# Optimization experiments

Measured on AMD Instinct MI355X. Metric: run time of the kernel, lower is better.

Reference implementation:

```python
import jax, jax.numpy as jnp
import numpy as np

C = 256          # in_dim
DQK = C // 16    # query/key channels after 1x1 conv


def setup_inputs() -> dict:
    key = jax.random.key(0)
    ks = jax.random.split(key, 10)
    B, W, H = 8, 64, 64
    s = 0.02
    return {
        "x1": jax.random.normal(ks[0], (B, C, W, H), jnp.float32),
        "x2": jax.random.normal(ks[1], (B, C, W, H), jnp.float32),
        "Wq": jax.random.normal(ks[2], (DQK, 2 * C), jnp.float32) * s,
        "bq": jnp.zeros((DQK,), jnp.float32),
        "Wk": jax.random.normal(ks[3], (DQK, 2 * C), jnp.float32) * s,
        "bk": jnp.zeros((DQK,), jnp.float32),
        "Wv1": jax.random.normal(ks[4], (C, C), jnp.float32) * s,
        "bv1": jnp.zeros((C,), jnp.float32),
        "Wv2": jax.random.normal(ks[5], (C, C), jnp.float32) * s,
        "bv2": jnp.zeros((C,), jnp.float32),
    }


def reference(x1, x2, Wq, bq, Wk, bk, Wv1, bv1, Wv2, bv2):
    B, c, W, H = x1.shape
    N = W * H
    x = jnp.concatenate([x1, x2], axis=1)            # [B, 2C, W, H]
    xf = x.reshape(B, 2 * c, N)                      # flatten spatial
    # 1x1 convs == channel matmuls
    q = jnp.einsum('dc,bcn->bnd', Wq, xf) + bq       # [B, N, DQK]
    k = jnp.einsum('dc,bcn->bdn', Wk, xf) + bk[None, :, None]  # [B, DQK, N]
    energy = jnp.einsum('bnd,bdm->bnm', q, k)        # [B, N, N]
    attention = jax.nn.softmax(energy, axis=-1)
    x1f = x1.reshape(B, c, N)
    x2f = x2.reshape(B, c, N)
    v1 = jnp.einsum('oc,bcn->bon', Wv1, x1f) + bv1[None, :, None]
    v2 = jnp.einsum('oc,bcn->bon', Wv2, x2f) + bv2[None, :, None]
    # bmm(value, attention^T): out[b,c,n] = sum_m v[b,c,m] * attention[b,n,m]
    out1 = jnp.einsum('bcm,bnm->bcn', v1, attention).reshape(B, c, W, H) + x1
    out2 = jnp.einsum('bcm,bnm->bcn', v2, attention).reshape(B, c, W, H) + x2
    return out1, out2, attention
```

## Files before the change

### kernel.cpp

```cpp
#include <hip/hip_runtime.h>
#include <hip/hip_bf16.h>

#define B_ 8
#define C_ 256
#define N_ 4096
#define D_ 16
#define TWO_C 512

#define PSLOT_SHORTS 4128
#define PSLOT_BYTES  (PSLOT_SHORTS * 2)

typedef __bf16 bf16x8 __attribute__((ext_vector_type(8)));
typedef __bf16 bf16x4 __attribute__((ext_vector_type(4)));
typedef float f32x4 __attribute__((ext_vector_type(4)));
typedef unsigned short u16x4 __attribute__((ext_vector_type(4)));

static __device__ __forceinline__ unsigned short f2bf_rtn(float f) {
    unsigned int u = __builtin_bit_cast(unsigned int, f);
    u += 0x7fffu + ((u >> 16) & 1u);
    return (unsigned short)(u >> 16);
}

static __device__ __forceinline__ float bf2f(unsigned short s) {
    return __builtin_bit_cast(float, (unsigned int)s << 16);
}

__device__ __forceinline__ void gld16(const void* g, void* l) {
    __builtin_amdgcn_global_load_lds(
        (const __attribute__((address_space(1))) unsigned int*)g,
        (__attribute__((address_space(3))) unsigned int*)l, 16, 0, 0);
}

__device__ __forceinline__ f32x4 expv(f32x4 e) {
    f32x4 r = { __expf(e[0]), __expf(e[1]), __expf(e[2]), __expf(e[3]) };
    return r;
}

#define MF(K, Q) __builtin_amdgcn_mfma_f32_16x16x32_bf16((K), (Q), zerov, 0, 0, 0)

__global__ __launch_bounds__(256) void wconv(
    const float* __restrict__ Wv1, const float* __restrict__ Wv2,
    unsigned short* __restrict__ Wbf)
{
    const int i = blockIdx.x * 256 + threadIdx.x;
    f32x4 a = ((const f32x4*)Wv1)[i];
    f32x4 b = ((const f32x4*)Wv2)[i];
    u16x4 ua = { f2bf_rtn(a[0]), f2bf_rtn(a[1]), f2bf_rtn(a[2]), f2bf_rtn(a[3]) };
    u16x4 ub = { f2bf_rtn(b[0]), f2bf_rtn(b[1]), f2bf_rtn(b[2]), f2bf_rtn(b[3]) };
    ((u16x4*)Wbf)[i] = ua;
    ((u16x4*)Wbf)[16384 + i] = ub;
}

__global__ __launch_bounds__(256) void qk_part(
    const float* __restrict__ x1, const float* __restrict__ x2,
    const float* __restrict__ Wq, const float* __restrict__ Wk,
    float* __restrict__ pq, float* __restrict__ pk,
    unsigned short* __restrict__ xbfT)
{
    const int tid = threadIdx.x;
    const int bid = blockIdx.x;
    const int ch = bid & 3;
    const int nt = (bid >> 2) & 15;
    const int b  = bid >> 6;
    const int n  = nt * 256 + tid;

    const float* xs  = (ch < 2) ? x1 : x2;
    const int xoff = (ch & 1) * 128;
    const int wcol = ch * 128;

    const float* px = xs + ((size_t)b * C_ + xoff) * N_ + n;
    unsigned short* xT = xbfT + ((size_t)b * N_ + n) * TWO_C + wcol;

    float aq[D_], ak[D_];
#pragma unroll
    for (int d = 0; d < D_; ++d) { aq[d] = 0.f; ak[d] = 0.f; }

    for (int c8 = 0; c8 < 16; ++c8) {
        unsigned short xb[8];
#pragma unroll
        for (int j = 0; j < 8; ++j) {
            const int c = c8 * 8 + j;
            float xv = px[(size_t)c * N_];
            xb[j] = f2bf_rtn(xv);
#pragma unroll
            for (int d = 0; d < D_; ++d) {
                aq[d] += Wq[d * TWO_C + wcol + c] * xv;
                ak[d] += Wk[d * TWO_C + wcol + c] * xv;
            }
        }
        u16x4 lo = { xb[0], xb[1], xb[2], xb[3] };
        u16x4 hi = { xb[4], xb[5], xb[6], xb[7] };
        *(u16x4*)(xT + c8 * 8)     = lo;
        *(u16x4*)(xT + c8 * 8 + 4) = hi;
    }

    f32x4* q4 = (f32x4*)pq + (size_t)ch * B_ * N_ * 4 + ((size_t)b * N_ + n) * 4;
    f32x4* k4 = (f32x4*)pk + (size_t)ch * B_ * N_ * 4 + ((size_t)b * N_ + n) * 4;
#pragma unroll
    for (int j = 0; j < 4; ++j) {
        f32x4 tq = { aq[4*j], aq[4*j+1], aq[4*j+2], aq[4*j+3] };
        f32x4 tk = { ak[4*j], ak[4*j+1], ak[4*j+2], ak[4*j+3] };
        q4[j] = tq;
        k4[j] = tk;
    }
}

__global__ __launch_bounds__(256) void qk_reduce(
    const float* __restrict__ pq, const float* __restrict__ pk,
    const float* __restrict__ bq, const float* __restrict__ bk,
    unsigned short* __restrict__ qbf, unsigned short* __restrict__ kbf)
{
    const int tg = blockIdx.x * 256 + threadIdx.x;
    const int row = tg >> 2;
    const int d4  = tg & 3;
    const f32x4* pq4 = (const f32x4*)pq;
    const f32x4* pk4 = (const f32x4*)pk;
    f32x4 q = ((const f32x4*)bq)[d4];
    f32x4 k = ((const f32x4*)bk)[d4];
    const size_t stride = (size_t)B_ * N_ * 4;
#pragma unroll
    for (int ch = 0; ch < 4; ++ch) {
        q += pq4[ch * stride + tg];
        k += pk4[ch * stride + tg];
    }
    u16x4 qo = { f2bf_rtn(q[0]), f2bf_rtn(q[1]), f2bf_rtn(q[2]), f2bf_rtn(q[3]) };
    u16x4 ko = { f2bf_rtn(k[0]), f2bf_rtn(k[1]), f2bf_rtn(k[2]), f2bf_rtn(k[3]) };
    u16x4 z  = { 0, 0, 0, 0 };
    *(u16x4*)(qbf + (size_t)row * 32 + d4 * 4)      = qo;
    *(u16x4*)(qbf + (size_t)row * 32 + 16 + d4 * 4) = z;
    *(u16x4*)(kbf + (size_t)row * 32 + d4 * 4)      = ko;
    *(u16x4*)(kbf + (size_t)row * 32 + 16 + d4 * 4) = z;
}

__global__ __launch_bounds__(256) void v_mfma(
    const unsigned short* __restrict__ Wbf,
    const unsigned short* __restrict__ xbfT,
    const float* __restrict__ bv1, const float* __restrict__ bv2,
    unsigned short* __restrict__ vstack)
{
    const int tid  = threadIdx.x;
    const int lane = tid & 63;
    const int wid  = tid >> 6;
    const int bid  = blockIdx.x;
    const int b    = bid >> 7;
    const int half = (bid >> 6) & 1;
    const int n0   = (bid & 63) * 64;
    const int col  = lane & 15;
    const int grp  = lane >> 4;
    const int koff = grp * 8;

    const unsigned short* pa[4];
    const unsigned short* pb[4];
#pragma unroll
    for (int ai = 0; ai < 4; ++ai)
        pa[ai] = Wbf + (size_t)(half * 256 + wid * 64 + ai * 16 + col) * 256 + koff;
#pragma unroll
    for (int bj = 0; bj < 4; ++bj)
        pb[bj] = xbfT + ((size_t)b * N_ + n0 + bj * 16 + col) * TWO_C + half * 256 + koff;

    f32x4 acc[4][4];
#pragma unroll
    for (int ai = 0; ai < 4; ++ai)
#pragma unroll
        for (int bj = 0; bj < 4; ++bj)
            acc[ai][bj] = (f32x4){0.f, 0.f, 0.f, 0.f};

#pragma unroll
    for (int s = 0; s < 8; ++s) {
        bf16x8 af[4], bfr[4];
#pragma unroll
        for (int ai = 0; ai < 4; ++ai) af[ai] = *(const bf16x8*)(pa[ai] + s * 32);
#pragma unroll
        for (int bj = 0; bj < 4; ++bj) bfr[bj] = *(const bf16x8*)(pb[bj] + s * 32);
#pragma unroll
        for (int ai = 0; ai < 4; ++ai)
#pragma unroll
            for (int bj = 0; bj < 4; ++bj)
                acc[ai][bj] = __builtin_amdgcn_mfma_f32_16x16x32_bf16(
                    af[ai], bfr[bj], acc[ai][bj], 0, 0, 0);
    }

    const float* bias = half ? bv2 : bv1;
#pragma unroll
    for (int ai = 0; ai < 4; ++ai) {
        const int cb = wid * 64 + ai * 16 + grp * 4;
#pragma unroll
        for (int r = 0; r < 4; ++r) {
            const float bv = bias[cb + r];
            unsigned short* vr = vstack + ((size_t)b * 512 + half * 256 + cb + r) * N_;
#pragma unroll
            for (int bj = 0; bj < 4; ++bj)
                vr[n0 + bj * 16 + col] = f2bf_rtn(acc[ai][bj][r] + bv);
        }
    }
}

__global__ __launch_bounds__(256) void rowsum(
    const unsigned short* __restrict__ qbf,
    const unsigned short* __restrict__ kbf,
    float* __restrict__ sinvbuf)
{
    const int tid  = threadIdx.x;
    const int lane = tid & 63;
    const int wid  = tid >> 6;
    const int b  = blockIdx.x >> 6;
    const int n0 = (blockIdx.x & 63) * 64 + wid * 16;
    const int col = lane & 15;
    const int grp = lane >> 4;
    const f32x4 zerov = {0.f, 0.f, 0.f, 0.f};

    const bf16x8 qf = *(const bf16x8*)(qbf + ((size_t)b * N_ + n0 + col) * 32 + grp * 8);
    const unsigned short* kp = kbf + ((size_t)b * N_ + col) * 32 + grp * 8;

    float rs = 0.f;
#pragma unroll 4
    for (int t = 0; t < 128; ++t) {
        bf16x8 k0 = *(const bf16x8*)kp;
        bf16x8 k1 = *(const bf16x8*)(kp + 512);
        kp += 1024;
        f32x4 p0 = expv(MF(k0, qf));
        f32x4 p1 = expv(MF(k1, qf));
        rs += (p0[0] + p0[1]) + (p0[2] + p0[3])
            + (p1[0] + p1[1]) + (p1[2] + p1[3]);
    }
    rs += __shfl_xor(rs, 16);
    rs += __shfl_xor(rs, 32);
    if (lane < 16)
        sinvbuf[(size_t)b * N_ + n0 + col] = 1.f / rs;
}

__global__ __launch_bounds__(512) void fused_pv(
    const unsigned short* __restrict__ qbf,
    const unsigned short* __restrict__ kbf,
    const unsigned short* __restrict__ vstack,
    const float* __restrict__ sinvbuf,
    const float* __restrict__ x1, const float* __restrict__ x2,
    float* __restrict__ out1, float* __restrict__ out2,
    float* __restrict__ att)
{
    __shared__ unsigned short AsmR[3][256 * 32];
    __shared__ unsigned short Bring[3][PSLOT_SHORTS];
    __shared__ float sinvLds[128];

    const int tid  = threadIdx.x;
    const int lane = tid & 63;
    const int wid  = tid >> 6;
    const int wr   = wid >> 2;
    const int wc   = wid & 3;
    const int col  = lane & 15;
    const int grp  = lane >> 4;

    const int bid  = blockIdx.x;
    const int orig = (bid & 7) * 64 + (bid >> 3);
    const int b   = orig >> 6;
    const int idx = orig & 63;
    const int ct  = idx & 1;
    const int nt  = idx >> 1;
    const int n0  = nt * 128;

    const f32x4 zerov = {0.f, 0.f, 0.f, 0.f};

    const int nl = wid * 16 + col;
    if (tid < 128) sinvLds[tid] = sinvbuf[(size_t)b * N_ + n0 + tid];

    const bf16x8 qf = *(const bf16x8*)(qbf + ((size_t)b * N_ + n0 + nl) * 32 + grp * 8);
    const unsigned short* kbase = kbf + ((size_t)b * N_ + col) * 32 + grp * 8;

    const unsigned short* Vb = vstack + ((size_t)b * 512 + ct * 256) * N_;
    const int q1 = tid + 512;
    const unsigned short* pa0g = Vb + (size_t)(tid >> 2) * N_ + (((tid & 3) ^ ((tid >> 2) & 3)) * 8);
    const unsigned short* pa1g = Vb + (size_t)(q1 >> 2) * N_ + (((q1 & 3) ^ ((q1 >> 2) & 3)) * 8);

    const int bwA = nl * 64 + ((((grp >> 1)) ^ (col & 3)) << 4) + (grp & 1) * 8;
    const int bwB = bwA ^ 32;

    const int raBase = (wr * 128 + col) * 64 + ((grp ^ (col & 3)) << 4);
    const int rbBase = (wc * 32  + col) * 64 + ((grp ^ (col & 3)) << 4);

    const int fj = lane >> 3;
    const int fu = (lane >> 1) & 3;
    const int fh = lane & 1;
    const int rlF = ct * 64 + wid * 8 + fj;
    const int flOff = rlF * 64 + ((fu ^ (fj & 3)) << 4) + fh * 8;
    float* const attF = att + (size_t)b * N_ * N_ + (size_t)(n0 + rlF) * N_ + (lane & 7) * 4;

    f32x4 acc[8][2];
#pragma unroll
    for (int ai = 0; ai < 8; ++ai)
#pragma unroll
        for (int bj = 0; bj < 2; ++bj)
            acc[ai][bj] = zerov;

#define PACKB(P, BASE, OFF) do {                                              \
    bf16x4 pkv = { (__bf16)(P)[0], (__bf16)(P)[1],                            \
                   (__bf16)(P)[2], (__bf16)(P)[3] };                          \
    *(bf16x4*)((char*)(BASE) + (OFF)) = pkv;                                  \
} while (0)

    unsigned short *aC = &AsmR[0][0], *aN = &AsmR[1][0], *aT = &AsmR[2][0];
    unsigned short *pPrev = &Bring[2][0], *pC = &Bring[0][0], *pN = &Bring[1][0];

    gld16(pa0g, aC + tid * 8);
    gld16(pa1g, aC + tid * 8 + 4096);
    gld16(pa0g + 32, aN + tid * 8);
    gld16(pa1g + 32, aN + tid * 8 + 4096);
    __builtin_amdgcn_sched_barrier(0);
    bf16x8 kA0, kA1, kB0, kB1;
    kA0 = *(const bf16x8*)kbase;
    kA1 = *(const bf16x8*)(kbase + 512);
    kB0 = *(const bf16x8*)(kbase + 1024);
    kB1 = *(const bf16x8*)(kbase + 1536);
    {
        f32x4 p0 = expv(MF(kA0, qf));
        f32x4 p1 = expv(MF(kA1, qf));
        PACKB(p0, pC, bwA);
        PACKB(p1, pC, bwB);
    }
    asm volatile("s_waitcnt lgkmcnt(0)" ::: "memory");
    __builtin_amdgcn_s_barrier();
    __builtin_amdgcn_sched_barrier(0);
    const float ivF = sinvLds[rlF];

    auto step = [&](const bf16x8& kc0, const bf16x8& kc1,
                    bf16x8& kn0, bf16x8& kn1, int T) {
        bf16x8 bfr[2], af0[4], af1[4];
#pragma unroll
        for (int bj = 0; bj < 2; ++bj)
            bfr[bj] = *(const bf16x8*)((const char*)pC + rbBase + bj * 1024);
#pragma unroll
        for (int ai = 0; ai < 4; ++ai)
            af0[ai] = *(const bf16x8*)((const char*)aC + raBase + ai * 1024);
        const int mt2 = (T + 2 < 128) ? T + 2 : 127;
        gld16(pa0g + (size_t)mt2 * 32, aT + tid * 8);
        gld16(pa1g + (size_t)mt2 * 32, aT + tid * 8 + 4096);
        __builtin_amdgcn_sched_barrier(0);
        {
            f32x4 e0 = MF(kc0, qf);
            f32x4 e1 = MF(kc1, qf);
            kn0 = *(const bf16x8*)(kbase + (size_t)mt2 * 1024);
            kn1 = *(const bf16x8*)(kbase + (size_t)mt2 * 1024 + 512);
            f32x4 p0 = expv(e0);
            f32x4 p1 = expv(e1);
            PACKB(p0, pN, bwA);
            PACKB(p1, pN, bwB);
        }
        if (T > 0) {
            u16x4 pb = *(const u16x4*)((const char*)pPrev + flOff);
            f32x4 pv = { bf2f(pb[0]) * ivF, bf2f(pb[1]) * ivF,
                         bf2f(pb[2]) * ivF, bf2f(pb[3]) * ivF };
            *(f32x4*)(attF + (size_t)(T - 1) * 32) = pv;
        }
#pragma unroll
        for (int ai = 0; ai < 4; ++ai)
#pragma unroll
            for (int bj = 0; bj < 2; ++bj)
                acc[ai][bj] = __builtin_amdgcn_mfma_f32_16x16x32_bf16(
                    af0[ai], bfr[bj], acc[ai][bj], 0, 0, 0);
#pragma unroll
        for (int ai = 0; ai < 4; ++ai)
            af1[ai] = *(const bf16x8*)((const char*)aC + raBase + (4 + ai) * 1024);
#pragma unroll
        for (int ai = 0; ai < 4; ++ai)
#pragma unroll
            for (int bj = 0; bj < 2; ++bj)
                acc[4 + ai][bj] = __builtin_amdgcn_mfma_f32_16x16x32_bf16(
                    af1[ai], bfr[bj], acc[4 + ai][bj], 0, 0, 0);
        asm volatile("s_waitcnt lgkmcnt(0)" ::: "memory");
        __builtin_amdgcn_s_barrier();
        __builtin_amdgcn_sched_barrier(0);
        unsigned short* t1 = aC; aC = aN; aN = aT; aT = t1;
        unsigned short* t2 = pPrev; pPrev = pC; pC = pN; pN = t2;
    };

    for (int tt = 0; tt < 64; ++tt) {
        step(kB0, kB1, kA0, kA1, 2 * tt);
        step(kA0, kA1, kB0, kB1, 2 * tt + 1);
    }

    {
        u16x4 pb = *(const u16x4*)((const char*)pPrev + flOff);
        f32x4 pv = { bf2f(pb[0]) * ivF, bf2f(pb[1]) * ivF,
                     bf2f(pb[2]) * ivF, bf2f(pb[3]) * ivF };
        *(f32x4*)(attF + (size_t)127 * 32) = pv;
    }

    float* outp     = ct ? out2 : out1;
    const float* xp = ct ? x2 : x1;
    float sc[2];
#pragma unroll
    for (int bj = 0; bj < 2; ++bj)
        sc[bj] = sinvLds[wc * 32 + bj * 16 + col];
#pragma unroll
    for (int ai = 0; ai < 8; ++ai) {
        const int c_l = wr * 128 + ai * 16 + grp * 4;
#pragma unroll
        for (int bj = 0; bj < 2; ++bj) {
            const int n = n0 + wc * 32 + bj * 16 + col;
#pragma unroll
            for (int r = 0; r < 4; ++r) {
                const size_t idx = ((size_t)b * C_ + c_l + r) * N_ + n;
                outp[idx] = acc[ai][bj][r] * sc[bj] + xp[idx];
            }
        }
    }
#undef PACKB
}

extern "C" void kernel_launch(void* const* d_in, const int* in_sizes, int n_in,
                              void* d_out, int out_size, void* d_ws, size_t ws_size,
                              hipStream_t stream)
{
    const float* x1  = (const float*)d_in[0];
    const float* x2  = (const float*)d_in[1];
    const float* Wq  = (const float*)d_in[2];
    const float* bq  = (const float*)d_in[3];
    const float* Wk  = (const float*)d_in[4];
    const float* bk  = (const float*)d_in[5];
    const float* Wv1 = (const float*)d_in[6];
    const float* bv1 = (const float*)d_in[7];
    const float* Wv2 = (const float*)d_in[8];
    const float* bv2 = (const float*)d_in[9];

    float* out  = (float*)d_out;
    float* out1 = out;
    float* out2 = out + (size_t)B_ * C_ * N_;
    float* att  = out + 2 * (size_t)B_ * C_ * N_;

    unsigned short* xbfT = (unsigned short*)att;

    char* ws = (char*)d_ws;
    unsigned short* qbf = (unsigned short*)ws;
    unsigned short* kbf = (unsigned short*)(ws + (size_t)2 * 1024 * 1024);
    unsigned short* vstack = (unsigned short*)(ws + (size_t)4 * 1024 * 1024);
    float* pq = (float*)(ws + (size_t)36 * 1024 * 1024);
    float* pk = (float*)(ws + (size_t)44 * 1024 * 1024);
    unsigned short* Wbf = (unsigned short*)(ws + (size_t)52 * 1024 * 1024);
    float* sinvbuf = (float*)(ws + (size_t)53 * 1024 * 1024);

    wconv<<<64, 256, 0, stream>>>(Wv1, Wv2, Wbf);
    qk_part<<<B_ * 16 * 4, 256, 0, stream>>>(x1, x2, Wq, Wk, pq, pk, xbfT);
    qk_reduce<<<(B_ * N_ * 4) / 256, 256, 0, stream>>>(pq, pk, bq, bk, qbf, kbf);
    rowsum<<<B_ * 64, 256, 0, stream>>>(qbf, kbf, sinvbuf);
    v_mfma<<<B_ * 2 * 64, 256, 0, stream>>>(Wbf, xbfT, bv1, bv2, vstack);
    fused_pv<<<512, 512, 0, stream>>>(qbf, kbf, vstack, sinvbuf, x1, x2, out1, out2, att);
}
```

Before: 507.1 us.

## Double query tile per block to 256 rows and batch attention stores

Each fused_pv block now covers 256 query positions instead of 128, so every V tile loaded from global is reused across twice as many outputs, and the grid shrinks from 512 to 256 blocks. The P ring grows to six slots, and attention-matrix writes are batched every four steps from older slots, giving wider, more coalesced stores. The cost is a larger accumulator array (32 MFMA tiles per wave), more LDS, and fewer blocks than the 256 CUs can absorb, so occupancy and latency hiding may suffer.

After: 481.5 us. 1.05x faster.

```diff
diff --git a/kernel.cpp b/kernel.cpp
--- a/kernel.cpp
+++ b/kernel.cpp
@@ -7,8 +7,9 @@
 #define D_ 16
 #define TWO_C 512
 
-#define PSLOT_SHORTS 4128
-#define PSLOT_BYTES  (PSLOT_SHORTS * 2)
+#define ASB 16384
+#define PSLOT_SHORTS 8224
+#define PSB (PSLOT_SHORTS*2)
 
 typedef __bf16 bf16x8 __attribute__((ext_vector_type(8)));
 typedef __bf16 bf16x4 __attribute__((ext_vector_type(4)));
@@ -238,9 +239,9 @@
     float* __restrict__ out1, float* __restrict__ out2,
     float* __restrict__ att)
 {
-    __shared__ unsigned short AsmR[3][256 * 32];
-    __shared__ unsigned short Bring[3][PSLOT_SHORTS];
-    __shared__ float sinvLds[128];
+    __shared__ unsigned short Ar[3 * (ASB / 2)];
+    __shared__ unsigned short Pr[6 * PSLOT_SHORTS];
+    __shared__ float sinvLds[256];
 
     const int tid  = threadIdx.x;
     const int lane = tid & 63;
@@ -251,19 +252,20 @@
     const int grp  = lane >> 4;
 
     const int bid  = blockIdx.x;
-    const int orig = (bid & 7) * 64 + (bid >> 3);
-    const int b   = orig >> 6;
-    const int idx = orig & 63;
+    const int orig = (bid & 7) * 32 + (bid >> 3);
+    const int b   = orig >> 5;
+    const int idx = orig & 31;
     const int ct  = idx & 1;
     const int nt  = idx >> 1;
-    const int n0  = nt * 128;
+    const int n0  = nt * 256;
 
     const f32x4 zerov = {0.f, 0.f, 0.f, 0.f};
 
     const int nl = wid * 16 + col;
-    if (tid < 128) sinvLds[tid] = sinvbuf[(size_t)b * N_ + n0 + tid];
-
-    const bf16x8 qf = *(const bf16x8*)(qbf + ((size_t)b * N_ + n0 + nl) * 32 + grp * 8);
+    if (tid < 256) sinvLds[tid] = sinvbuf[(size_t)b * N_ + n0 + tid];
+
+    const bf16x8 qf0 = *(const bf16x8*)(qbf + ((size_t)b * N_ + n0 + nl) * 32 + grp * 8);
+    const bf16x8 qf1 = *(const bf16x8*)(qbf + ((size_t)b * N_ + n0 + 128 + nl) * 32 + grp * 8);
     const unsigned short* kbase = kbf + ((size_t)b * N_ + col) * 32 + grp * 8;
 
     const unsigned short* Vb = vstack + ((size_t)b * 512 + ct * 256) * N_;
@@ -271,105 +273,135 @@
     const unsigned short* pa0g = Vb + (size_t)(tid >> 2) * N_ + (((tid & 3) ^ ((tid >> 2) & 3)) * 8);
     const unsigned short* pa1g = Vb + (size_t)(q1 >> 2) * N_ + (((q1 & 3) ^ ((q1 >> 2) & 3)) * 8);
 
-    const int bwA = nl * 64 + ((((grp >> 1)) ^ (col & 3)) << 4) + (grp & 1) * 8;
+    const int bwA = nl * 64 + ((((grp >> 1)) ^ (nl & 3)) << 4) + (grp & 1) * 8;
     const int bwB = bwA ^ 32;
 
-    const int raBase = (wr * 128 + col) * 64 + ((grp ^ (col & 3)) << 4);
-    const int rbBase = (wc * 32  + col) * 64 + ((grp ^ (col & 3)) << 4);
-
-    const int fj = lane >> 3;
-    const int fu = (lane >> 1) & 3;
-    const int fh = lane & 1;
-    const int rlF = ct * 64 + wid * 8 + fj;
-    const int flOff = rlF * 64 + ((fu ^ (fj & 3)) << 4) + fh * 8;
-    float* const attF = att + (size_t)b * N_ * N_ + (size_t)(n0 + rlF) * N_ + (lane & 7) * 4;
-
-    f32x4 acc[8][2];
+    int raOff[8], rbOff[4];
+#pragma unroll
+    for (int ai = 0; ai < 8; ++ai) {
+        const int ra = wr * 128 + ai * 16 + col;
+        raOff[ai] = ra * 64 + ((grp ^ (ra & 3)) << 4);
+    }
+#pragma unroll
+    for (int bj = 0; bj < 4; ++bj) {
+        const int rb = wc * 64 + bj * 16 + col;
+        rbOff[bj] = rb * 64 + ((grp ^ (rb & 3)) << 4);
+    }
+
+    const int rbase = ct * 128 + wid * 16;
+    const int l31   = lane & 31;
+    const int twB   = (l31 >> 3) * PSB;
+    const int ul    = (lane & 7) >> 1;
+    const int fh    = lane & 1;
+    float* const attL = att + (size_t)b * N_ * N_ + (size_t)n0 * N_ + l31 * 4;
+
+    f32x4 acc[8][4];
 #pragma unroll
     for (int ai = 0; ai < 8; ++ai)
 #pragma unroll
-        for (int bj = 0; bj < 2; ++bj)
+        for (int bj = 0; bj < 4; ++bj)
             acc[ai][bj] = zerov;
 
-#define PACKB(P, BASE, OFF) do {                                              \
+#define PACKB(P, OFF) do {                                                    \
     bf16x4 pkv = { (__bf16)(P)[0], (__bf16)(P)[1],                            \
                    (__bf16)(P)[2], (__bf16)(P)[3] };                          \
-    *(bf16x4*)((char*)(BASE) + (OFF)) = pkv;                                  \
+    *(bf16x4*)((char*)Pr + (OFF)) = pkv;                                      \
 } while (0)
 
-    unsigned short *aC = &AsmR[0][0], *aN = &AsmR[1][0], *aT = &AsmR[2][0];
-    unsigned short *pPrev = &Bring[2][0], *pC = &Bring[0][0], *pN = &Bring[1][0];
-
-    gld16(pa0g, aC + tid * 8);
-    gld16(pa1g, aC + tid * 8 + 4096);
-    gld16(pa0g + 32, aN + tid * 8);
-    gld16(pa1g + 32, aN + tid * 8 + 4096);
+    gld16(pa0g,      (char*)Ar + tid * 16);
+    gld16(pa1g,      (char*)Ar + 8192 + tid * 16);
+    gld16(pa0g + 32, (char*)Ar + ASB + tid * 16);
+    gld16(pa1g + 32, (char*)Ar + ASB + 8192 + tid * 16);
     __builtin_amdgcn_sched_barrier(0);
     bf16x8 kA0, kA1, kB0, kB1;
-    kA0 = *(const bf16x8*)kbase;
-    kA1 = *(const bf16x8*)(kbase + 512);
-    kB0 = *(const bf16x8*)(kbase + 1024);
-    kB1 = *(const bf16x8*)(kbase + 1536);
     {
-        f32x4 p0 = expv(MF(kA0, qf));
-        f32x4 p1 = expv(MF(kA1, qf));
-        PACKB(p0, pC, bwA);
-        PACKB(p1, pC, bwB);
-    }
-    asm volatile("s_waitcnt lgkmcnt(0)" ::: "memory");
+        bf16x8 k00 = *(const bf16x8*)kbase;
+        bf16x8 k01 = *(const bf16x8*)(kbase + 512);
+        kB0 = *(const bf16x8*)(kbase + 1024);
+        kB1 = *(const bf16x8*)(kbase + 1536);
+        f32x4 p00 = expv(MF(k00, qf0));
+        f32x4 p01 = expv(MF(k01, qf0));
+        f32x4 p10 = expv(MF(k00, qf1));
+        f32x4 p11 = expv(MF(k01, qf1));
+        PACKB(p00, bwA);
+        PACKB(p01, bwB);
+        PACKB(p10, bwA + 128 * 64);
+        PACKB(p11, bwB + 128 * 64);
+    }
+    asm volatile("s_waitcnt vmcnt(2) lgkmcnt(0)" ::: "memory");
     __builtin_amdgcn_s_barrier();
     __builtin_amdgcn_sched_barrier(0);
-    const float ivF = sinvLds[rlF];
+
+    int aCur = 0;
+    int pCur = 0;
 
     auto step = [&](const bf16x8& kc0, const bf16x8& kc1,
                     bf16x8& kn0, bf16x8& kn1, int T) {
-        bf16x8 bfr[2], af0[4], af1[4];
-#pragma unroll
-        for (int bj = 0; bj < 2; ++bj)
-            bfr[bj] = *(const bf16x8*)((const char*)pC + rbBase + bj * 1024);
+        bf16x8 bfr[4], af0[4], af1[4];
+#pragma unroll
+        for (int bj = 0; bj < 4; ++bj)
+            bfr[bj] = *(const bf16x8*)((const char*)Pr + pCur + rbOff[bj]);
 #pragma unroll
         for (int ai = 0; ai < 4; ++ai)
-            af0[ai] = *(const bf16x8*)((const char*)aC + raBase + ai * 1024);
-        const int mt2 = (T + 2 < 128) ? T + 2 : 127;
-        gld16(pa0g + (size_t)mt2 * 32, aT + tid * 8);
-        gld16(pa1g + (size_t)mt2 * 32, aT + tid * 8 + 4096);
+            af0[ai] = *(const bf16x8*)((const char*)Ar + aCur + raOff[ai]);
+        if (T < 126) {
+            int aStage = aCur + 2 * ASB; if (aStage >= 3 * ASB) aStage -= 3 * ASB;
+            gld16(pa0g + (size_t)(T + 2) * 32, (char*)Ar + aStage + tid * 16);
+            gld16(pa1g + (size_t)(T + 2) * 32, (char*)Ar + aStage + 8192 + tid * 16);
+        }
         __builtin_amdgcn_sched_barrier(0);
-        {
-            f32x4 e0 = MF(kc0, qf);
-            f32x4 e1 = MF(kc1, qf);
-            kn0 = *(const bf16x8*)(kbase + (size_t)mt2 * 1024);
-            kn1 = *(const bf16x8*)(kbase + (size_t)mt2 * 1024 + 512);
-            f32x4 p0 = expv(e0);
-            f32x4 p1 = expv(e1);
-            PACKB(p0, pN, bwA);
-            PACKB(p1, pN, bwB);
-        }
-        if (T > 0) {
-            u16x4 pb = *(const u16x4*)((const char*)pPrev + flOff);
-            f32x4 pv = { bf2f(pb[0]) * ivF, bf2f(pb[1]) * ivF,
-                         bf2f(pb[2]) * ivF, bf2f(pb[3]) * ivF };
-            *(f32x4*)(attF + (size_t)(T - 1) * 32) = pv;
+        if (T < 127) {
+            f32x4 e00 = MF(kc0, qf0);
+            f32x4 e01 = MF(kc1, qf0);
+            f32x4 e10 = MF(kc0, qf1);
+            f32x4 e11 = MF(kc1, qf1);
+            if (T < 126) {
+                kn0 = *(const bf16x8*)(kbase + (size_t)(T + 2) * 1024);
+                kn1 = *(const bf16x8*)(kbase + (size_t)(T + 2) * 1024 + 512);
+            }
+            int pNxt = pCur + PSB; if (pNxt >= 6 * PSB) pNxt = 0;
+            f32x4 p00 = expv(e00), p01 = expv(e01);
+            f32x4 p10 = expv(e10), p11 = expv(e11);
+            PACKB(p00, pNxt + bwA);
+            PACKB(p01, pNxt + bwB);
+            PACKB(p10, pNxt + bwA + 128 * 64);
+            PACKB(p11, pNxt + bwB + 128 * 64);
+        }
+        if ((T & 3) == 0 && T >= 4) {
+            int fB = pCur - 4 * PSB; if (fB < 0) fB += 6 * PSB;
+            int sB = fB + twB; if (sB >= 6 * PSB) sB -= 6 * PSB;
+            const int W0m = (T - 4) * 32;
+#pragma unroll
+            for (int i = 0; i < 8; ++i) {
+                const int r  = rbase + 2 * i + (lane >> 5);
+                const int sw = ((ul ^ (r & 3)) << 4) + fh * 8;
+                u16x4 pb = *(const u16x4*)((const char*)Pr + sB + r * 64 + sw);
+                const float iv = sinvLds[r];
+                f32x4 pv = { bf2f(pb[0]) * iv, bf2f(pb[1]) * iv,
+                             bf2f(pb[2]) * iv, bf2f(pb[3]) * iv };
+                *(f32x4*)(attL + (size_t)r * N_ + W0m) = pv;
+            }
         }
 #pragma unroll
         for (int ai = 0; ai < 4; ++ai)
 #pragma unroll
-            for (int bj = 0; bj < 2; ++bj)
+            for (int bj = 0; bj < 4; ++bj)
                 acc[ai][bj] = __builtin_amdgcn_mfma_f32_16x16x32_bf16(
                     af0[ai], bfr[bj], acc[ai][bj], 0, 0, 0);
 #pragma unroll
         for (int ai = 0; ai < 4; ++ai)
-            af1[ai] = *(const bf16x8*)((const char*)aC + raBase + (4 + ai) * 1024);
+            af1[ai] = *(const bf16x8*)((const char*)Ar + aCur + raOff[4 + ai]);
 #pragma unroll
         for (int ai = 0; ai < 4; ++ai)
 #pragma unroll
-            for (int bj = 0; bj < 2; ++bj)
+            for (int bj = 0; bj < 4; ++bj)
                 acc[4 + ai][bj] = __builtin_amdgcn_mfma_f32_16x16x32_bf16(
                     af1[ai], bfr[bj], acc[4 + ai][bj], 0, 0, 0);
         asm volatile("s_waitcnt lgkmcnt(0)" ::: "memory");
         __builtin_amdgcn_s_barrier();
         __builtin_amdgcn_sched_barrier(0);
-        unsigned short* t1 = aC; aC = aN; aN = aT; aT = t1;
-        unsigned short* t2 = pPrev; pPrev = pC; pC = pN; pN = t2;
+        aCur += ASB; if (aCur == 3 * ASB) aCur = 0;
+        pCur += PSB; if (pCur == 6 * PSB) pCur = 0;
     };
 
     for (int tt = 0; tt < 64; ++tt) {
@@ -378,28 +410,36 @@
     }
 
     {
-        u16x4 pb = *(const u16x4*)((const char*)pPrev + flOff);
-        f32x4 pv = { bf2f(pb[0]) * ivF, bf2f(pb[1]) * ivF,
-                     bf2f(pb[2]) * ivF, bf2f(pb[3]) * ivF };
-        *(f32x4*)(attF + (size_t)127 * 32) = pv;
+        int fB = pCur - 4 * PSB; if (fB < 0) fB += 6 * PSB;
+        int sB = fB + twB; if (sB >= 6 * PSB) sB -= 6 * PSB;
+#pragma unroll
+        for (int i = 0; i < 8; ++i) {
+            const int r  = rbase + 2 * i + (lane >> 5);
+            const int sw = ((ul ^ (r & 3)) << 4) + fh * 8;
+            u16x4 pb = *(const u16x4*)((const char*)Pr + sB + r * 64 + sw);
+            const float iv = sinvLds[r];
+            f32x4 pv = { bf2f(pb[0]) * iv, bf2f(pb[1]) * iv,
+                         bf2f(pb[2]) * iv, bf2f(pb[3]) * iv };
+            *(f32x4*)(attL + (size_t)r * N_ + 124 * 32) = pv;
+        }
     }
 
     float* outp     = ct ? out2 : out1;
     const float* xp = ct ? x2 : x1;
-    float sc[2];
-#pragma unroll
-    for (int bj = 0; bj < 2; ++bj)
-        sc[bj] = sinvLds[wc * 32 + bj * 16 + col];
+    float sc[4];
+#pragma unroll
+    for (int bj = 0; bj < 4; ++bj)
+        sc[bj] = sinvLds[wc * 64 + bj * 16 + col];
 #pragma unroll
     for (int ai = 0; ai < 8; ++ai) {
         const int c_l = wr * 128 + ai * 16 + grp * 4;
 #pragma unroll
-        for (int bj = 0; bj < 2; ++bj) {
-            const int n = n0 + wc * 32 + bj * 16 + col;
+        for (int bj = 0; bj < 4; ++bj) {
+            const int n = n0 + wc * 64 + bj * 16 + col;
 #pragma unroll
             for (int r = 0; r < 4; ++r) {
-                const size_t idx = ((size_t)b * C_ + c_l + r) * N_ + n;
-                outp[idx] = acc[ai][bj][r] * sc[bj] + xp[idx];
+                const size_t idx2 = ((size_t)b * C_ + c_l + r) * N_ + n;
+                outp[idx2] = acc[ai][bj][r] * sc[bj] + xp[idx2];
             }
         }
     }
@@ -442,5 +482,5 @@
     qk_reduce<<<(B_ * N_ * 4) / 256, 256, 0, stream>>>(pq, pk, bq, bk, qbf, kbf);
     rowsum<<<B_ * 64, 256, 0, stream>>>(qbf, kbf, sinvbuf);
     v_mfma<<<B_ * 2 * 64, 256, 0, stream>>>(Wbf, xbfT, bv1, bv2, vstack);
-    fused_pv<<<512, 512, 0, stream>>>(qbf, kbf, vstack, sinvbuf, x1, x2, out1, out2, att);
-}
+    fused_pv<<<256, 512, 0, stream>>>(qbf, kbf, vstack, sinvbuf, x1, x2, out1, out2, att);
+}
```
